# Kernel optimization log

Measured on AMD Instinct MI355X. Metric: run time of the kernel, lower is better.

## Reference

```python
import jax, jax.numpy as jnp
import numpy as np

ALPHAS = (0.1, 0.3, 0.5)
WEIGHTS = (0.5, 0.3, 0.2)

B, T, D = 32, 8192, 64


def setup_inputs() -> dict:
    key = jax.random.key(0)
    k1, k2 = jax.random.split(key)
    pred = jax.random.normal(k1, (B, T, D), dtype=jnp.float32)
    target = jax.random.normal(k2, (B, T, D), dtype=jnp.float32)
    return {"pred": pred, "target": target}


def _ema(x, alpha):
    # ema_0 = x_0 ; ema_i = alpha*x_i + (1-alpha)*ema_{i-1}
    # Express each step as affine op (mult, add) and compose with an
    # associative scan along the time axis (dim=1):  y_i = mult*y_{i-1} + add.
    mult = jnp.full(x.shape, 1.0 - alpha, dtype=x.dtype).at[:, 0].set(0.0)
    add = (alpha * x).at[:, 0].set(x[:, 0])

    def combine(c1, c2):  # apply c1 first, then c2
        a1, b1 = c1
        a2, b2 = c2
        return (a1 * a2, b1 * a2 + b2)

    _, ema = jax.lax.associative_scan(combine, (mult, add), axis=1)
    return ema


def _scale_loss(pred, target, alpha):
    pe = _ema(pred, alpha)   # [B, T, D]
    te = _ema(target, alpha)
    pd = pe[:, 1:] - pe[:, :-1]
    td = te[:, 1:] - te[:, :-1]
    mismatch = jnp.sign(pd) != jnp.sign(td)
    step_err = jnp.square(pe[:, 1:] - te[:, 1:])
    masked = jnp.where(mismatch, step_err, jnp.zeros_like(step_err))
    return masked.mean(axis=1)  # [B, D]


def reference(pred, target):
    loss = sum(w * _scale_loss(pred, target, a) for a, w in zip(ALPHAS, WEIGHTS))
    return loss.mean()  # reduction='mean'
```

## Files before the change

### kernel.cpp

```cpp
#include <hip/hip_runtime.h>


namespace {
constexpr int BB  = 32;
constexpr int TT  = 8192;
constexpr int DD  = 64;
constexpr int CH  = 64;
constexpr int WU  = 32;
constexpr int NCH = TT / CH;
constexpr int WPB = 4;
constexpr int BT  = 8;
constexpr float INV_NORM = 1.0f / (8191.0f * 2048.0f);
}

typedef const __attribute__((address_space(1))) void* gas_ptr;
typedef __attribute__((address_space(3))) void* las_ptr;

__global__ void zero_out_kernel(float* o) { o[0] = 0.0f; }

#define WAIT_V4() do { asm volatile("s_waitcnt vmcnt(4)" ::: "memory"); \
                       __builtin_amdgcn_sched_barrier(0); } while (0)
#define WAIT_V0() do { asm volatile("s_waitcnt vmcnt(0)" ::: "memory"); \
                       __builtin_amdgcn_sched_barrier(0); } while (0)
#define WAIT_LG() do { asm volatile("s_waitcnt lgkmcnt(0)" ::: "memory"); \
                       __builtin_amdgcn_sched_barrier(0); } while (0)

__device__ __forceinline__ void issue_batch(const float* gx, const float* gy,
                                            float* lx, float* ly) {
#pragma unroll
  for (int r = 0; r < 2; ++r) {
    __builtin_amdgcn_global_load_lds((gas_ptr)(gx + r * 4 * DD),
                                     (las_ptr)(lx + r * 4 * DD), 16, 0, 0);
    __builtin_amdgcn_global_load_lds((gas_ptr)(gy + r * 4 * DD),
                                     (las_ptr)(ly + r * 4 * DD), 16, 0, 0);
  }
}

__device__ __forceinline__ void warm8_a0(const float* tx, const float* ty,
                                         float& pe0, float& te0) {
#pragma unroll
  for (int i = 0; i < BT; ++i) {
    float xx = tx[i * DD], yy = ty[i * DD];
    pe0 = fmaf(0.1f, xx - pe0, pe0);
    te0 = fmaf(0.1f, yy - te0, te0);
  }
}

__device__ __forceinline__ void warm8_all(const float* tx, const float* ty,
    float& pe0, float& te0, float& pe1, float& te1, float& pe2, float& te2) {
#pragma unroll
  for (int i = 0; i < BT; ++i) {
    float xx = tx[i * DD], yy = ty[i * DD];
    pe0 = fmaf(0.1f, xx - pe0, pe0);  te0 = fmaf(0.1f, yy - te0, te0);
    pe1 = fmaf(0.3f, xx - pe1, pe1);  te1 = fmaf(0.3f, yy - te1, te1);
    pe2 = fmaf(0.5f, xx - pe2, pe2);  te2 = fmaf(0.5f, yy - te2, te2);
  }
}

__device__ __forceinline__ void step1(float xx, float yy, float a, float w,
                                      float& pe, float& te, float& acc) {
  float dx = xx - pe;
  float dy = yy - te;
  pe = fmaf(a, dx, pe);
  te = fmaf(a, dy, te);
  float e   = pe - te;
  float sel = (dx * dy < 0.0f) ? w : 0.0f;
  acc = fmaf(sel, e * e, acc);
}

__device__ __forceinline__ void acc8(const float* tx, const float* ty,
    float& pe0, float& te0, float& pe1, float& te1, float& pe2, float& te2,
    float& acc) {
#pragma unroll
  for (int i = 0; i < BT; ++i) {
    float xx = tx[i * DD], yy = ty[i * DD];
    step1(xx, yy, 0.1f, 0.5f, pe0, te0, acc);
    step1(xx, yy, 0.3f, 0.3f, pe1, te1, acc);
    step1(xx, yy, 0.5f, 0.2f, pe2, te2, acc);
  }
}

__global__ void __launch_bounds__(256)
ms_trend_loss_kernel(const float* __restrict__ pred,
                     const float* __restrict__ targ,
                     float* __restrict__ out) {
  const int lane = threadIdx.x & 63;
  const int wave = threadIdx.x >> 6;
  const int unit = blockIdx.x * WPB + wave;
  const int b = unit >> 7;
  const int c = unit & 127;
  const int s = c * CH;
  const int start = (c == 0) ? 0 : (s - WU);

  const float* gx = pred + (b * TT + start) * DD + lane * 4;
  const float* gy = targ + (b * TT + start) * DD + lane * 4;

  __shared__ float tile[WPB][2][2][BT * DD];
#define LX(k) (&tile[wave][(k) & 1][0][0])
#define LY(k) (&tile[wave][(k) & 1][1][0])
#define TX(k) (&tile[wave][(k) & 1][0][lane])
#define TY(k) (&tile[wave][(k) & 1][1][lane])

  float pe0, pe1, pe2, te0, te1, te2;
  float acc = 0.0f;

  issue_batch(gx, gy, LX(0), LY(0));
  issue_batch(gx + BT * DD, gy + BT * DD, LX(1), LY(1));

  if (c == 0) {
    WAIT_V4();
    pe0 = pe1 = pe2 = TX(0)[0];
    te0 = te1 = te2 = TY(0)[0];
    acc8(TX(0), TY(0), pe0, te0, pe1, te1, pe2, te2, acc);
    WAIT_LG();
    issue_batch(gx + 2 * BT * DD, gy + 2 * BT * DD, LX(0), LY(0));
    for (int k = 1; k < 6; ++k) {
      WAIT_V4();
      acc8(TX(k), TY(k), pe0, te0, pe1, te1, pe2, te2, acc);
      WAIT_LG();
      issue_batch(gx + (k + 2) * BT * DD, gy + (k + 2) * BT * DD, LX(k), LY(k));
    }
    WAIT_V4();
    acc8(TX(6), TY(6), pe0, te0, pe1, te1, pe2, te2, acc);
    WAIT_V0();
    acc8(TX(7), TY(7), pe0, te0, pe1, te1, pe2, te2, acc);
  } else {
    WAIT_V4();
    pe0 = TX(0)[0];
    te0 = TY(0)[0];
    warm8_a0(TX(0), TY(0), pe0, te0);
    WAIT_LG();
    issue_batch(gx + 2 * BT * DD, gy + 2 * BT * DD, LX(0), LY(0));
    WAIT_V4();
    warm8_a0(TX(1), TY(1), pe0, te0);
    WAIT_LG();
    issue_batch(gx + 3 * BT * DD, gy + 3 * BT * DD, LX(1), LY(1));
    WAIT_V4();
    pe1 = pe2 = TX(2)[0];
    te1 = te2 = TY(2)[0];
    warm8_all(TX(2), TY(2), pe0, te0, pe1, te1, pe2, te2);
    WAIT_LG();
    issue_batch(gx + 4 * BT * DD, gy + 4 * BT * DD, LX(2), LY(2));
    WAIT_V4();
    warm8_all(TX(3), TY(3), pe0, te0, pe1, te1, pe2, te2);
    WAIT_LG();
    issue_batch(gx + 5 * BT * DD, gy + 5 * BT * DD, LX(3), LY(3));
    for (int k = 4; k < 10; ++k) {
      WAIT_V4();
      acc8(TX(k), TY(k), pe0, te0, pe1, te1, pe2, te2, acc);
      WAIT_LG();
      issue_batch(gx + (k + 2) * BT * DD, gy + (k + 2) * BT * DD, LX(k), LY(k));
    }
    WAIT_V4();
    acc8(TX(10), TY(10), pe0, te0, pe1, te1, pe2, te2, acc);
    WAIT_V0();
    acc8(TX(11), TY(11), pe0, te0, pe1, te1, pe2, te2, acc);
  }

#pragma unroll
  for (int off = 32; off > 0; off >>= 1) acc += __shfl_down(acc, off);
  __shared__ float sred[WPB];
  if (lane == 0) sred[wave] = acc;
  __syncthreads();
  if (threadIdx.x == 0) {
    float t = sred[0] + sred[1] + sred[2] + sred[3];
    atomicAdd(out, t * INV_NORM);
  }
}

extern "C" void kernel_launch(void* const* d_in, const int* in_sizes, int n_in,
                              void* d_out, int out_size, void* d_ws, size_t ws_size,
                              hipStream_t stream) {
  (void)in_sizes; (void)n_in; (void)out_size; (void)d_ws; (void)ws_size;
  const float* pred = (const float*)d_in[0];
  const float* targ = (const float*)d_in[1];
  float* out = (float*)d_out;

  zero_out_kernel<<<1, 1, 0, stream>>>(out);
  ms_trend_loss_kernel<<<BB * NCH / WPB, 256, 0, stream>>>(pred, targ, out);
}
```

Measured before the change: 157.3 us.

## Use longer time chunks with a triple-buffered LDS load ring

Each wave now handles 256 timesteps instead of 64, so the 32-step warm-up overlap is recomputed for fewer chunks and less redundant data is loaded. Loads move to 16-row batches through a three-slot LDS ring, with two batches in flight, using a generic loop in place of the hand-unrolled schedule, and blocks shrink to two waves. Only 1024 waves are launched, which cuts parallelism and latency hiding on a large GPU. The runtime-branched loop may also add scheduling overhead.

```diff
diff --git a/kernel.cpp b/kernel.cpp
--- a/kernel.cpp
+++ b/kernel.cpp
@@ -5,11 +5,12 @@
 constexpr int BB  = 32;
 constexpr int TT  = 8192;
 constexpr int DD  = 64;
-constexpr int CH  = 64;
+constexpr int CH  = 256;
 constexpr int WU  = 32;
 constexpr int NCH = TT / CH;
-constexpr int WPB = 4;
-constexpr int BT  = 8;
+constexpr int WPB = 2;
+constexpr int BT  = 16;
+constexpr int NBUF = 3;
 constexpr float INV_NORM = 1.0f / (8191.0f * 2048.0f);
 }
 
@@ -18,26 +19,24 @@
 
 __global__ void zero_out_kernel(float* o) { o[0] = 0.0f; }
 
-#define WAIT_V4() do { asm volatile("s_waitcnt vmcnt(4)" ::: "memory"); \
-                       __builtin_amdgcn_sched_barrier(0); } while (0)
-#define WAIT_V0() do { asm volatile("s_waitcnt vmcnt(0)" ::: "memory"); \
-                       __builtin_amdgcn_sched_barrier(0); } while (0)
-#define WAIT_LG() do { asm volatile("s_waitcnt lgkmcnt(0)" ::: "memory"); \
-                       __builtin_amdgcn_sched_barrier(0); } while (0)
+#define SBAR() __builtin_amdgcn_sched_barrier(0)
+#define WAIT_V8() do { asm volatile("s_waitcnt vmcnt(8)" ::: "memory"); SBAR(); } while (0)
+#define WAIT_V0() do { asm volatile("s_waitcnt vmcnt(0)" ::: "memory"); SBAR(); } while (0)
 
 __device__ __forceinline__ void issue_batch(const float* gx, const float* gy,
                                             float* lx, float* ly) {
 #pragma unroll
-  for (int r = 0; r < 2; ++r) {
+  for (int r = 0; r < 4; ++r) {
     __builtin_amdgcn_global_load_lds((gas_ptr)(gx + r * 4 * DD),
                                      (las_ptr)(lx + r * 4 * DD), 16, 0, 0);
     __builtin_amdgcn_global_load_lds((gas_ptr)(gy + r * 4 * DD),
                                      (las_ptr)(ly + r * 4 * DD), 16, 0, 0);
   }
+  SBAR();
 }
 
-__device__ __forceinline__ void warm8_a0(const float* tx, const float* ty,
-                                         float& pe0, float& te0) {
+__device__ __forceinline__ void warm16_a0_t(const float* tx, const float* ty,
+                                            float& pe0, float& te0) {
 #pragma unroll
   for (int i = 0; i < BT; ++i) {
     float xx = tx[i * DD], yy = ty[i * DD];
@@ -46,7 +45,7 @@
   }
 }
 
-__device__ __forceinline__ void warm8_all(const float* tx, const float* ty,
+__device__ __forceinline__ void warm16_all_t(const float* tx, const float* ty,
     float& pe0, float& te0, float& pe1, float& te1, float& pe2, float& te2) {
 #pragma unroll
   for (int i = 0; i < BT; ++i) {
@@ -68,7 +67,7 @@
   acc = fmaf(sel, e * e, acc);
 }
 
-__device__ __forceinline__ void acc8(const float* tx, const float* ty,
+__device__ __forceinline__ void acc16_t(const float* tx, const float* ty,
     float& pe0, float& te0, float& pe1, float& te1, float& pe2, float& te2,
     float& acc) {
 #pragma unroll
@@ -80,81 +79,55 @@
   }
 }
 
-__global__ void __launch_bounds__(256)
+__global__ void __launch_bounds__(128)
 ms_trend_loss_kernel(const float* __restrict__ pred,
                      const float* __restrict__ targ,
                      float* __restrict__ out) {
   const int lane = threadIdx.x & 63;
   const int wave = threadIdx.x >> 6;
   const int unit = blockIdx.x * WPB + wave;
-  const int b = unit >> 7;
-  const int c = unit & 127;
-  const int s = c * CH;
-  const int start = (c == 0) ? 0 : (s - WU);
+  const int b = unit >> 5;
+  const int c = unit & 31;
+  const int start = (c == 0) ? 0 : (c * CH - WU);
+  const int nb = (c == 0) ? (CH / BT) : ((CH + WU) / BT);
 
   const float* gx = pred + (b * TT + start) * DD + lane * 4;
   const float* gy = targ + (b * TT + start) * DD + lane * 4;
 
-  __shared__ float tile[WPB][2][2][BT * DD];
-#define LX(k) (&tile[wave][(k) & 1][0][0])
-#define LY(k) (&tile[wave][(k) & 1][1][0])
-#define TX(k) (&tile[wave][(k) & 1][0][lane])
-#define TY(k) (&tile[wave][(k) & 1][1][lane])
+  __shared__ float tile[WPB][NBUF][2][BT * DD];
 
-  float pe0, pe1, pe2, te0, te1, te2;
+  float pe0 = 0.f, pe1 = 0.f, pe2 = 0.f, te0 = 0.f, te1 = 0.f, te2 = 0.f;
   float acc = 0.0f;
 
-  issue_batch(gx, gy, LX(0), LY(0));
-  issue_batch(gx + BT * DD, gy + BT * DD, LX(1), LY(1));
+  issue_batch(gx,           gy,           &tile[wave][0][0][0], &tile[wave][0][1][0]);
+  issue_batch(gx + BT * DD, gy + BT * DD, &tile[wave][1][0][0], &tile[wave][1][1][0]);
 
-  if (c == 0) {
-    WAIT_V4();
-    pe0 = pe1 = pe2 = TX(0)[0];
-    te0 = te1 = te2 = TY(0)[0];
-    acc8(TX(0), TY(0), pe0, te0, pe1, te1, pe2, te2, acc);
-    WAIT_LG();
-    issue_batch(gx + 2 * BT * DD, gy + 2 * BT * DD, LX(0), LY(0));
-    for (int k = 1; k < 6; ++k) {
-      WAIT_V4();
-      acc8(TX(k), TY(k), pe0, te0, pe1, te1, pe2, te2, acc);
-      WAIT_LG();
-      issue_batch(gx + (k + 2) * BT * DD, gy + (k + 2) * BT * DD, LX(k), LY(k));
+  int rb = 0;
+  for (int k = 0; k < nb; ++k) {
+    if (k < nb - 1) { WAIT_V8(); } else { WAIT_V0(); }
+    const float* tx = &tile[wave][rb][0][lane];
+    const float* ty = &tile[wave][rb][1][lane];
+    if (c == 0) {
+      if (k == 0) { pe0 = pe1 = pe2 = tx[0]; te0 = te1 = te2 = ty[0]; }
+      acc16_t(tx, ty, pe0, te0, pe1, te1, pe2, te2, acc);
+    } else {
+      if (k == 0) {
+        pe0 = tx[0]; te0 = ty[0];
+        warm16_a0_t(tx, ty, pe0, te0);
+      } else if (k == 1) {
+        pe1 = pe2 = tx[0]; te1 = te2 = ty[0];
+        warm16_all_t(tx, ty, pe0, te0, pe1, te1, pe2, te2);
+      } else {
+        acc16_t(tx, ty, pe0, te0, pe1, te1, pe2, te2, acc);
+      }
     }
-    WAIT_V4();
-    acc8(TX(6), TY(6), pe0, te0, pe1, te1, pe2, te2, acc);
-    WAIT_V0();
-    acc8(TX(7), TY(7), pe0, te0, pe1, te1, pe2, te2, acc);
-  } else {
-    WAIT_V4();
-    pe0 = TX(0)[0];
-    te0 = TY(0)[0];
-    warm8_a0(TX(0), TY(0), pe0, te0);
-    WAIT_LG();
-    issue_batch(gx + 2 * BT * DD, gy + 2 * BT * DD, LX(0), LY(0));
-    WAIT_V4();
-    warm8_a0(TX(1), TY(1), pe0, te0);
-    WAIT_LG();
-    issue_batch(gx + 3 * BT * DD, gy + 3 * BT * DD, LX(1), LY(1));
-    WAIT_V4();
-    pe1 = pe2 = TX(2)[0];
-    te1 = te2 = TY(2)[0];
-    warm8_all(TX(2), TY(2), pe0, te0, pe1, te1, pe2, te2);
-    WAIT_LG();
-    issue_batch(gx + 4 * BT * DD, gy + 4 * BT * DD, LX(2), LY(2));
-    WAIT_V4();
-    warm8_all(TX(3), TY(3), pe0, te0, pe1, te1, pe2, te2);
-    WAIT_LG();
-    issue_batch(gx + 5 * BT * DD, gy + 5 * BT * DD, LX(3), LY(3));
-    for (int k = 4; k < 10; ++k) {
-      WAIT_V4();
-      acc8(TX(k), TY(k), pe0, te0, pe1, te1, pe2, te2, acc);
-      WAIT_LG();
-      issue_batch(gx + (k + 2) * BT * DD, gy + (k + 2) * BT * DD, LX(k), LY(k));
+    SBAR();
+    if (k + 2 < nb) {
+      int ib = rb + 2; if (ib >= NBUF) ib -= NBUF;
+      issue_batch(gx + (k + 2) * BT * DD, gy + (k + 2) * BT * DD,
+                  &tile[wave][ib][0][0], &tile[wave][ib][1][0]);
     }
-    WAIT_V4();
-    acc8(TX(10), TY(10), pe0, te0, pe1, te1, pe2, te2, acc);
-    WAIT_V0();
-    acc8(TX(11), TY(11), pe0, te0, pe1, te1, pe2, te2, acc);
+    rb = (rb + 1 == NBUF) ? 0 : rb + 1;
   }
 
 #pragma unroll
@@ -163,7 +136,7 @@
   if (lane == 0) sred[wave] = acc;
   __syncthreads();
   if (threadIdx.x == 0) {
-    float t = sred[0] + sred[1] + sred[2] + sred[3];
+    float t = sred[0] + sred[1];
     atomicAdd(out, t * INV_NORM);
   }
 }
@@ -177,5 +150,5 @@
   float* out = (float*)d_out;
 
   zero_out_kernel<<<1, 1, 0, stream>>>(out);
-  ms_trend_loss_kernel<<<BB * NCH / WPB, 256, 0, stream>>>(pred, targ, out);
+  ms_trend_loss_kernel<<<BB * NCH / WPB, WPB * 64, 0, stream>>>(pred, targ, out);
 }
```

Measured after the change: 153.3 us. 1.03x faster.
